# Kernel tuning notes

Hardware: AMD Instinct MI355X
Metric: run time of the kernel (lower is better)

Reference implementation:

```python
import jax, jax.numpy as jnp
import numpy as np

MODES = 32
NUM_BLOCKS = 4
NUM_EXPERTS = 16
TOP_K = 4
TEMPERATURE = 2.0


def _gelu(t):
    return jax.nn.gelu(t, approximate=False)  # torch F.gelu default (erf)


def _c1(x, w, b):
    # 1x1 conv: x [B,C,H,W], w [O,C], b [O]
    return jnp.einsum('bchw,oc->bohw', x, w) + b[None, :, None, None]


def _group_norm(x, w, b, groups=8, eps=1e-5):
    B, C, H, W = x.shape
    xg = x.reshape(B, groups, C // groups, H, W)
    mu = xg.mean(axis=(2, 3, 4), keepdims=True)
    var = xg.var(axis=(2, 3, 4), keepdims=True)
    xn = ((xg - mu) * jax.lax.rsqrt(var + eps)).reshape(B, C, H, W)
    return xn * w[None, :, None, None] + b[None, :, None, None]


def _bn_eval(x, g, b, rm, rv, eps=1e-5):
    # eval-mode BatchNorm with running stats
    return (x - rm) * jax.lax.rsqrt(rv + eps) * g + b


def _afno(x, w1, b1, w2, b2):
    # x: [B,C,H,W] (channel_first). Block-diagonal complex MLP on low FFT modes.
    B, C, H, W = x.shape
    bs = C // NUM_BLOCKS
    xp = x.transpose(0, 2, 3, 1)                      # [B,H,W,C]
    xf = jnp.fft.rfft2(xp, axes=(1, 2), norm='ortho') # [B,H,Wf,C] complex64
    Wf = xf.shape[2]
    xf = xf.reshape(B, H, Wf, NUM_BLOCKS, bs)
    m = MODES
    xm = xf[:, :m, :m]                                # kept modes only
    xr, xi = xm.real, xm.imag
    o1r = _gelu(jnp.einsum('bhwni,nio->bhwno', xr, w1[0])
                - jnp.einsum('bhwni,nio->bhwno', xi, w1[1]) + b1[0])
    o1i = _gelu(jnp.einsum('bhwni,nio->bhwno', xi, w1[0])
                + jnp.einsum('bhwni,nio->bhwno', xr, w1[1]) + b1[1])
    o2r = (jnp.einsum('bhwni,nio->bhwno', o1r, w2[0])
           - jnp.einsum('bhwni,nio->bhwno', o1i, w2[1]) + b2[0])
    o2i = (jnp.einsum('bhwni,nio->bhwno', o1i, w2[0])
           + jnp.einsum('bhwni,nio->bhwno', o1r, w2[1]) + b2[1])
    of = jnp.zeros((B, H, Wf, NUM_BLOCKS, bs), dtype=xf.dtype)
    of = of.at[:, :m, :m].set(o2r + 1j * o2i)
    out = jnp.fft.irfft2(of.reshape(B, H, Wf, C), s=(H, W), axes=(1, 2), norm='ortho')
    out = out + xp
    return out.transpose(0, 3, 1, 2)


def _forward(x, gn1_w, gn1_b, afno_w1, afno_b1, afno_w2, afno_b2,
             gn2_w, gn2_b, fe_w, fe_b, g1_w, g1_b, bn1_g, bn1_b, bn1_rm, bn1_rv,
             ca_w1, ca_b1, ca_w2, ca_b2, g2_w, g2_b, bn2_g, bn2_b, bn2_rm, bn2_rv,
             g3_w, g3_b, shared_w, shared_b, expert_w, expert_b):
    residual = x
    h = _group_norm(x, gn1_w, gn1_b)
    h = _afno(h, afno_w1, afno_b1, afno_w2, afno_b2)
    h = h + residual            # double_skip
    residual = h
    h = _group_norm(h, gn2_w, gn2_b)
    # MoEImage (eval mode -> loss_gate = 0)
    feats = _gelu(_c1(h, fe_w, fe_b))
    shared = jnp.zeros_like(h)
    for s in range(shared_w.shape[0]):
        shared = shared + _gelu(_c1(feats, shared_w[s], shared_b[s])) / shared_w.shape[0]
    # gating on global-avg-pooled features (1x1 convs == linears)
    gf = feats.mean(axis=(2, 3))                              # [B,C]
    h1 = _gelu(_bn_eval(gf @ g1_w.T + g1_b, bn1_g, bn1_b, bn1_rm, bn1_rv))
    a = _gelu(h1 @ ca_w1.T + ca_b1) @ ca_w2.T + ca_b2
    h1 = h1 * jax.nn.sigmoid(2.0 * a)                          # avg==max pool on 1x1 map
    h2 = _gelu(_bn_eval(h1 @ g2_w.T + g2_b, bn2_g, bn2_b, bn2_rm, bn2_rv))
    scores = h2 @ g3_w.T + g3_b                                # [B,E]
    vals, idx = jax.lax.top_k(scores, TOP_K)
    wts = jax.nn.softmax(vals / TEMPERATURE, axis=1)
    B = x.shape[0]
    gate_w = jnp.zeros((B, NUM_EXPERTS), x.dtype).at[jnp.arange(B)[:, None], idx].add(wts)
    out = shared
    for e in range(NUM_EXPERTS):
        out = out + _gelu(_c1(feats, expert_w[e], expert_b[e])) * gate_w[:, e][:, None, None, None]
    return out + residual


def setup_inputs():
    key = jax.random.key(0)
    ks = jax.random.split(key, 16)
    B, C, H, W = 8, 64, 192, 192
    nb = NUM_BLOCKS
    bs = C // nb
    E = NUM_EXPERTS
    scale = 1.0 / (bs * bs)
    f32 = jnp.float32
    n = lambda k, shape: jax.random.normal(k, shape, f32) * 0.02
    return {
        'x': jax.random.normal(ks[0], (B, C, H, W), f32),
        'gn1_w': jnp.ones((C,), f32), 'gn1_b': jnp.zeros((C,), f32),
        'afno_w1': jax.random.uniform(ks[1], (2, nb, bs, bs), f32) * scale,
        'afno_b1': jax.random.uniform(ks[2], (2, nb, bs), f32) * scale,
        'afno_w2': jax.random.uniform(ks[3], (2, nb, bs, bs), f32) * scale,
        'afno_b2': jax.random.uniform(ks[4], (2, nb, bs), f32) * scale,
        'gn2_w': jnp.ones((C,), f32), 'gn2_b': jnp.zeros((C,), f32),
        'fe_w': n(ks[5], (C, C)), 'fe_b': jnp.zeros((C,), f32),
        'g1_w': n(ks[6], (2 * C, C)), 'g1_b': jnp.zeros((2 * C,), f32),
        'bn1_g': jnp.ones((2 * C,), f32), 'bn1_b': jnp.zeros((2 * C,), f32),
        'bn1_rm': jnp.zeros((2 * C,), f32), 'bn1_rv': jnp.ones((2 * C,), f32),
        'ca_w1': n(ks[7], (2 * C // 16, 2 * C)), 'ca_b1': jnp.zeros((2 * C // 16,), f32),
        'ca_w2': n(ks[8], (2 * C, 2 * C // 16)), 'ca_b2': jnp.zeros((2 * C,), f32),
        'g2_w': n(ks[9], (C, 2 * C)), 'g2_b': jnp.zeros((C,), f32),
        'bn2_g': jnp.ones((C,), f32), 'bn2_b': jnp.zeros((C,), f32),
        'bn2_rm': jnp.zeros((C,), f32), 'bn2_rv': jnp.ones((C,), f32),
        'g3_w': n(ks[10], (E, C)), 'g3_b': jnp.zeros((E,), f32),
        'shared_w': n(ks[11], (2, C, C)), 'shared_b': jnp.zeros((2, C), f32),
        'expert_w': n(ks[12], (E, C, C)), 'expert_b': jnp.zeros((E, C), f32),
    }


def reference(x, gn1_w, gn1_b, afno_w1, afno_b1, afno_w2, afno_b2,
              gn2_w, gn2_b, fe_w, fe_b, g1_w, g1_b, bn1_g, bn1_b, bn1_rm, bn1_rv,
              ca_w1, ca_b1, ca_w2, ca_b2, g2_w, g2_b, bn2_g, bn2_b, bn2_rm, bn2_rv,
              g3_w, g3_b, shared_w, shared_b, expert_w, expert_b):
    return _forward(x, gn1_w, gn1_b, afno_w1, afno_b1, afno_w2, afno_b2,
                    gn2_w, gn2_b, fe_w, fe_b, g1_w, g1_b, bn1_g, bn1_b, bn1_rm, bn1_rv,
                    ca_w1, ca_b1, ca_w2, ca_b2, g2_w, g2_b, bn2_g, bn2_b, bn2_rm, bn2_rv,
                    g3_w, g3_b, shared_w, shared_b, expert_w, expert_b)
```

## Files before the change

kernel.cpp:

```cpp
#include <hip/hip_runtime.h>
#include <math.h>

#define TPI 6.283185307179586f

typedef __attribute__((ext_vector_type(8))) short bf8v;
typedef __attribute__((ext_vector_type(4))) float f4v;

#define MFMA(a,b,c) __builtin_amdgcn_mfma_f32_16x16x32_bf16((a),(b),(c),0,0,0)

__device__ __forceinline__ float gelu_f(float v){
  return 0.5f*v*(1.0f+erff(v*0.7071067811865475f));
}
__device__ __forceinline__ float gelu_fast(float x){
  float x3=x*x*x;
  float y=fmaf(0.044715f,x3,x)*0.7978845608f;
  float e=__expf(2.0f*y);
  float th=1.0f-2.0f/(e+1.0f);
  return 0.5f*x*(1.0f+th);
}
__device__ __forceinline__ unsigned short f2b(float f){
  union{float f; unsigned u;} v; v.f=f;
  unsigned r=v.u + 0x7FFFu + ((v.u>>16)&1u);
  return (unsigned short)(r>>16);
}

__global__ __launch_bounds__(256) void prep(const float* __restrict__ shw, const float* __restrict__ exw,
    const float* __restrict__ shb, const float* __restrict__ exb, const float* __restrict__ few,
    unsigned short* __restrict__ T, unsigned short* __restrict__ wall, float* __restrict__ ball,
    unsigned short* __restrict__ wfe, float* __restrict__ gfp){
  const float a = TPI/192.0f;
  int stride=gridDim.x*256;
  for(int i=blockIdx.x*256+threadIdx.x; i<61440; i+=stride){
    float v;
    if(i<12288){
      int n1=i/192, w=i%192; int kw=n1>>1, c=n1&1;
      int m=(kw*w)%192; float cs,sn; sincosf((float)m*a,&sn,&cs);
      v = c ? -sn : cs;
    } else if(i<36864){
      int j=i-12288; int n1=j/384, k1=j%384; int kh=n1>>1, d=n1&1; int h=k1>>1, c=k1&1;
      int m=(kh*h)%192; float cs,sn; sincosf((float)m*a,&sn,&cs);
      float e = d ? (c ? cs : -sn) : (c ? sn : cs);
      v = e*(1.0f/192.0f);
    } else if(i<49152){
      int j=i-36864; int h=j/64, k1=j%64; int kh=k1>>1, c=k1&1;
      int m=(h*kh)%192; float cs,sn; sincosf((float)m*a,&sn,&cs);
      v = c ? sn : cs;
    } else {
      int j=i-49152; int w=j/64, k1=j%64; int kw=k1>>1, d=k1&1;
      float f = kw ? (2.0f/192.0f) : (1.0f/192.0f);
      int m=(w*kw)%192; float cs,sn; sincosf((float)m*a,&sn,&cs);
      v = d ? -f*sn : f*cs;
    }
    T[i]=f2b(v);
  }
  for(int i=blockIdx.x*256+threadIdx.x;i<73728;i+=stride) wall[i]=f2b(i<8192?shw[i]:exw[i-8192]);
  for(int i=blockIdx.x*256+threadIdx.x;i<1152;i+=stride)  ball[i]=(i<128)?shb[i]:exb[i-128];
  for(int i=blockIdx.x*256+threadIdx.x;i<4096;i+=stride)  wfe[i]=f2b(few[i]);
  for(int i=blockIdx.x*256+threadIdx.x;i<512;i+=stride)   gfp[i]=0.f;
}

__global__ void gn_finalize(const float* __restrict__ part, const float* __restrict__ gw,
                            const float* __restrict__ gb, float2* __restrict__ sb){
  int g=threadIdx.x; if(g>=64) return;
  float S=0,SS=0;
  for(int j=0;j<8;j++){ S+=part[(g*8+j)*2]; SS+=part[(g*8+j)*2+1]; }
  const float inv=1.0f/294912.0f;
  float mean=S*inv, var=SS*inv-mean*mean;
  float rstd=rsqrtf(var+1e-5f);
  int b=g>>3, gg=g&7;
  for(int k=0;k<8;k++){
    int c=gg*8+k;
    float sc=rstd*gw[c];
    sb[b*64+c]=make_float2(sc, gb[c]-mean*sc);
  }
}

__global__ __launch_bounds__(256) void fwd_dft(const float* __restrict__ x,
      const unsigned short* __restrict__ TBf1, const unsigned short* __restrict__ TBf2,
      float* __restrict__ Xm2, float* __restrict__ part1){
  __shared__ __align__(16) unsigned short ldsA[64*200];
  __shared__ __align__(16) float sX[2048];
  __shared__ float red[8];
  int t=threadIdx.x, bc=blockIdx.x;
  int wave=t>>6, l=t&63, lr=l&15, lg=l>>4;
  const float* xch = x + (size_t)bc*36864;
  for(int i=t;i<1536;i+=256){
    int row=i/24, chunk=i%24;
    *(uint4*)&ldsA[row*200 + chunk*8] = *(const uint4*)(TBf1 + row*192 + chunk*8);
  }
  __syncthreads();
  float s_=0.f, ss_=0.f;
  f4v acc1[3][4];
  for(int mt=0;mt<3;mt++){
    int m0=(wave+mt*4)*16;
    const float* xrow = xch + (m0+lr)*192 + lg*8;
    bf8v af[6];
    #pragma unroll
    for(int ks=0;ks<6;ks++){
      float4 u0=*(const float4*)(xrow+ks*32);
      float4 u1=*(const float4*)(xrow+ks*32+4);
      s_ += u0.x+u0.y+u0.z+u0.w+u1.x+u1.y+u1.z+u1.w;
      ss_+= u0.x*u0.x+u0.y*u0.y+u0.z*u0.z+u0.w*u0.w
           +u1.x*u1.x+u1.y*u1.y+u1.z*u1.z+u1.w*u1.w;
      bf8v a;
      a[0]=(short)f2b(u0.x); a[1]=(short)f2b(u0.y); a[2]=(short)f2b(u0.z); a[3]=(short)f2b(u0.w);
      a[4]=(short)f2b(u1.x); a[5]=(short)f2b(u1.y); a[6]=(short)f2b(u1.z); a[7]=(short)f2b(u1.w);
      af[ks]=a;
    }
    #pragma unroll
    for(int nt=0;nt<4;nt++){
      f4v acc={0.f,0.f,0.f,0.f};
      #pragma unroll
      for(int ks=0;ks<6;ks++){
        bf8v b=*(const bf8v*)&ldsA[(nt*16+lr)*200 + ks*32 + lg*8];
        acc=MFMA(af[ks],b,acc);
      }
      acc1[mt][nt]=acc;
    }
  }
  __syncthreads();
  for(int mt=0;mt<3;mt++){
    int m0=(wave+mt*4)*16;
    #pragma unroll
    for(int nt=0;nt<4;nt++){
      int n1=nt*16+lr; int kw=n1>>1, c=n1&1;
      #pragma unroll
      for(int reg=0;reg<4;reg++){
        int h=m0+4*lg+reg;
        ldsA[kw*392 + 2*h + c]=f2b(acc1[mt][nt][reg]);
      }
    }
  }
  __syncthreads();
  for(int pp=0;pp<2;pp++){
    int p=wave+pp*4;
    int m0=(p>>2)*16, n0=(p&3)*16;
    f4v acc={0.f,0.f,0.f,0.f};
    #pragma unroll
    for(int ks=0;ks<12;ks++){
      bf8v a=*(const bf8v*)&ldsA[(m0+lr)*392 + ks*32 + lg*8];
      bf8v b=*(const bf8v*)(TBf2 + (n0+lr)*384 + ks*32 + lg*8);
      acc=MFMA(a,b,acc);
    }
    int n1=n0+lr; int kh=n1>>1, d=n1&1;
    #pragma unroll
    for(int reg=0;reg<4;reg++){
      int kw=m0+4*lg+reg;
      sX[(kh*32+kw)*2 + d]=acc[reg];
    }
  }
  __syncthreads();
  float* dst=Xm2+(size_t)bc*2048;
  for(int i=t;i<512;i+=256) *(float4*)(dst+i*4)=*(const float4*)(sX+i*4);
  #pragma unroll
  for(int o=32;o>0;o>>=1){ s_+=__shfl_down(s_,o); ss_+=__shfl_down(ss_,o); }
  if(l==0){ red[wave]=s_; red[4+wave]=ss_; }
  __syncthreads();
  if(t==0){
    part1[bc*2]  =red[0]+red[1]+red[2]+red[3];
    part1[bc*2+1]=red[4]+red[5]+red[6]+red[7];
  }
}

__global__ __launch_bounds__(256) void mode_mlp(const float* __restrict__ Xm2, const float2* __restrict__ sb1,
    const float* __restrict__ w1, const float* __restrict__ b1,
    const float* __restrict__ w2, const float* __restrict__ b2,
    float* __restrict__ S2){
  __shared__ float w10[1024], w11[1024], w20[1024], w21[1024];
  __shared__ float b10[64], b11[64], b20[64], b21[64];
  __shared__ float2 sbl[64];
  __shared__ float xr[32][64], xi[32][64];
  __shared__ float o1r[32][64], o1i[32][64];
  int t=threadIdx.x;
  int b=blockIdx.x>>5, kh=blockIdx.x&31;
  for(int i=t;i<1024;i+=256){ w10[i]=w1[i]; w11[i]=w1[1024+i]; w20[i]=w2[i]; w21[i]=w2[1024+i]; }
  if(t<64){ b10[t]=b1[t]; b11[t]=b1[64+t]; b20[t]=b2[t]; b21[t]=b2[64+t]; sbl[t]=sb1[b*64+t]; }
  __syncthreads();
  for(int q=0;q<16;q++){
    int idx=q*256+t; int c=idx>>6, jj=idx&63;
    float2 s=sbl[c];
    float v=Xm2[((size_t)(b*64+c))*2048 + kh*64 + jj]*s.x;
    if(kh==0 && jj==0) v += 192.0f*s.y;
    if(jj&1) xi[jj>>1][c]=v; else xr[jj>>1][c]=v;
  }
  __syncthreads();
  int tl=t&63, n=tl>>4, o=tl&15, wb=n*256+o;
  #pragma unroll
  for(int it=0;it<8;it++){
    int kw=(t>>6)+it*4;
    float a_r=b10[tl], a_i=b11[tl];
    #pragma unroll
    for(int i=0;i<16;i++){
      float rr=xr[kw][n*16+i], im=xi[kw][n*16+i];
      float W0=w10[wb+i*16], W1=w11[wb+i*16];
      a_r=fmaf(rr,W0,fmaf(-im,W1,a_r));
      a_i=fmaf(im,W0,fmaf( rr,W1,a_i));
    }
    o1r[kw][tl]=gelu_f(a_r); o1i[kw][tl]=gelu_f(a_i);
  }
  __syncthreads();
  #pragma unroll
  for(int it=0;it<8;it++){
    int kw=(t>>6)+it*4;
    float c_r=b20[tl], c_i=b21[tl];
    #pragma unroll
    for(int i=0;i<16;i++){
      float rr=o1r[kw][n*16+i], im=o1i[kw][n*16+i];
      float W0=w20[wb+i*16], W1=w21[wb+i*16];
      c_r=fmaf(rr,W0,fmaf(-im,W1,c_r));
      c_i=fmaf(im,W0,fmaf( rr,W1,c_i));
    }
    xr[kw][tl]=c_r; xi[kw][tl]=c_i;
  }
  __syncthreads();
  for(int q=0;q<16;q++){
    int idx=q*256+t; int c=idx>>6, jj=idx&63;
    float v = (jj&1) ? xi[jj>>1][c] : xr[jj>>1][c];
    S2[((size_t)(b*64+c))*2048 + kh*64 + jj]=v;
  }
}

__global__ __launch_bounds__(256) void inv_dft(const float* __restrict__ S2,
      const unsigned short* __restrict__ TAi, const unsigned short* __restrict__ TBi,
      const float* __restrict__ x, const float2* __restrict__ sb,
      float* __restrict__ h2, float* __restrict__ part2){
  __shared__ __align__(16) unsigned short Bs[64*72];
  __shared__ __align__(16) unsigned short GL[192*72];
  __shared__ float red[8];
  int t=threadIdx.x, bc=blockIdx.x;
  int wave=t>>6, l=t&63, lr=l&15, lg=l>>4;
  const float* sp=S2+(size_t)bc*2048;
  for(int i=t;i<1024;i+=256){
    int kh=i>>5, kw=i&31;
    float Sr=sp[(kh*32+kw)*2], Si=sp[(kh*32+kw)*2+1];
    unsigned short br=f2b(Sr), bi_=f2b(Si), nbi=f2b(-Si);
    Bs[(2*kw+0)*72 + 2*kh+0]=br;
    Bs[(2*kw+0)*72 + 2*kh+1]=nbi;
    Bs[(2*kw+1)*72 + 2*kh+0]=bi_;
    Bs[(2*kw+1)*72 + 2*kh+1]=br;
  }
  __syncthreads();
  for(int mt=0;mt<3;mt++){
    int m0=(wave+mt*4)*16;
    bf8v a0=*(const bf8v*)(TAi + (m0+lr)*64 + lg*8);
    bf8v a1=*(const bf8v*)(TAi + (m0+lr)*64 + 32 + lg*8);
    #pragma unroll
    for(int nt=0;nt<4;nt++){
      f4v acc={0.f,0.f,0.f,0.f};
      bf8v b0=*(const bf8v*)&Bs[(nt*16+lr)*72 + lg*8];
      bf8v b1=*(const bf8v*)&Bs[(nt*16+lr)*72 + 32 + lg*8];
      acc=MFMA(a0,b0,acc); acc=MFMA(a1,b1,acc);
      #pragma unroll
      for(int reg=0;reg<4;reg++)
        GL[(m0+4*lg+reg)*72 + nt*16+lr]=f2b(acc[reg]);
    }
  }
  __syncthreads();
  float2 sv=sb[bc];
  float cA=sv.x+1.0f, cB=sv.y;
  asm volatile("" : "+v"(cA), "+v"(cB));
  const float* xch=x+(size_t)bc*36864;
  float* och=h2+(size_t)bc*36864;
  float s_=0.f, ss_=0.f;
  for(int mt=0;mt<3;mt++){
    int m0=(wave+mt*4)*16;
    bf8v a0=*(const bf8v*)&GL[(m0+lr)*72 + lg*8];
    bf8v a1=*(const bf8v*)&GL[(m0+lr)*72 + 32 + lg*8];
    for(int nt=0;nt<12;nt++){
      int n0=nt*16;
      f4v acc={0.f,0.f,0.f,0.f};
      bf8v b0=*(const bf8v*)(TBi + (n0+lr)*64 + lg*8);
      bf8v b1=*(const bf8v*)(TBi + (n0+lr)*64 + 32 + lg*8);
      acc=MFMA(a0,b0,acc); acc=MFMA(a1,b1,acc);
      int w=n0+lr;
      #pragma unroll
      for(int reg=0;reg<4;reg++){
        int h=m0+4*lg+reg;
        int ga=h*192+w;
        float xv=xch[ga];
        float val=acc[reg]+fmaf(cA,xv,cB);
        och[ga]=val;
        s_+=val; ss_+=val*val;
      }
    }
  }
  #pragma unroll
  for(int o=32;o>0;o>>=1){ s_+=__shfl_down(s_,o); ss_+=__shfl_down(ss_,o); }
  if(l==0){ red[wave]=s_; red[4+wave]=ss_; }
  __syncthreads();
  if(t==0){
    part2[bc*2]  =red[0]+red[1]+red[2]+red[3];
    part2[bc*2+1]=red[4]+red[5]+red[6]+red[7];
  }
}

__global__ __launch_bounds__(256) void feats_k(const float* __restrict__ h2, const float2* __restrict__ sb,
    const unsigned short* __restrict__ wfe, const float* __restrict__ feb,
    unsigned short* __restrict__ feats, float* __restrict__ gfp){
  __shared__ __align__(16) unsigned short A[128*72];
  __shared__ float sgf[64];
  int t=threadIdx.x;
  int blk=blockIdx.x, b=blk/288, tile=blk-b*288, hw0=tile*128;
  if(t<64) sgf[t]=0.f;
  for(int i=t;i<2048;i+=256){
    int c=i>>5, q=i&31;
    float2 s=sb[b*64+c];
    float4 v=*(const float4*)&h2[(size_t)(b*64+c)*36864 + hw0 + q*4];
    int px0=q*4, sw=((px0>>4)&3)<<3, cc=c^sw;
    A[(px0+0)*72+cc]=f2b(fmaf(v.x,s.x,s.y));
    A[(px0+1)*72+cc]=f2b(fmaf(v.y,s.x,s.y));
    A[(px0+2)*72+cc]=f2b(fmaf(v.z,s.x,s.y));
    A[(px0+3)*72+cc]=f2b(fmaf(v.w,s.x,s.y));
  }
  __syncthreads();
  int wave=t>>6, l=t&63, lr=l&15, lg=l>>4;
  int pxb=wave*32;
  bf8v af[2][2], bfv[4][2];
  #pragma unroll
  for(int fm=0;fm<2;fm++){
    int row=pxb+fm*16+lr, sw=((row>>4)&3)<<3;
    #pragma unroll
    for(int ks=0;ks<2;ks++) af[fm][ks]=*(const bf8v*)&A[row*72+((ks*32+lg*8)^sw)];
  }
  #pragma unroll
  for(int fn=0;fn<4;fn++)
    #pragma unroll
    for(int ks=0;ks<2;ks++)
      bfv[fn][ks]=*(const bf8v*)(wfe+(fn*16+lr)*64+ks*32+lg*8);
  float gsum[4]={0.f,0.f,0.f,0.f};
  #pragma unroll
  for(int fm=0;fm<2;fm++)
    #pragma unroll
    for(int fn=0;fn<4;fn++){
      f4v acc={0.f,0.f,0.f,0.f};
      acc=MFMA(af[fm][0],bfv[fn][0],acc);
      acc=MFMA(af[fm][1],bfv[fn][1],acc);
      int oc=fn*16+lr;
      float bs=feb[oc];
      #pragma unroll
      for(int r=0;r<4;r++){
        float g=gelu_f(acc[r]+bs);
        gsum[fn]+=g;
        int px=hw0+pxb+fm*16+4*lg+r;
        feats[(size_t)(b*36864+px)*64+oc]=f2b(g);
      }
    }
  #pragma unroll
  for(int fn=0;fn<4;fn++){
    float v=gsum[fn];
    v+=__shfl_xor(v,16); v+=__shfl_xor(v,32);
    if(lg==0) atomicAdd(&sgf[fn*16+lr], v);
  }
  __syncthreads();
  if(t<64) atomicAdd(&gfp[b*64+t], sgf[t]);
}

__global__ __launch_bounds__(128) void gating(const float* __restrict__ gfp,
  const float* __restrict__ g1w, const float* __restrict__ g1b,
  const float* __restrict__ bn1g, const float* __restrict__ bn1b, const float* __restrict__ bn1m, const float* __restrict__ bn1v,
  const float* __restrict__ cw1, const float* __restrict__ cb1, const float* __restrict__ cw2, const float* __restrict__ cb2,
  const float* __restrict__ g2w, const float* __restrict__ g2b,
  const float* __restrict__ bn2g, const float* __restrict__ bn2b, const float* __restrict__ bn2m, const float* __restrict__ bn2v,
  const float* __restrict__ g3w, const float* __restrict__ g3b, float2* __restrict__ act){
  __shared__ float gf[8][64];
  __shared__ float h1[8][128];
  __shared__ float a1[8][8];
  __shared__ float h2g[8][64];
  __shared__ float sc[8][16];
  int t=threadIdx.x;
  for(int i=t;i<512;i+=128) gf[i>>6][i&63]=gfp[i]*(1.0f/36864.0f);
  __syncthreads();
  for(int i=t;i<1024;i+=128){
    int b=i>>7, j=i&127;
    float s=g1b[j];
    for(int c=0;c<64;c++) s=fmaf(gf[b][c], g1w[j*64+c], s);
    s=(s-bn1m[j])*rsqrtf(bn1v[j]+1e-5f)*bn1g[j]+bn1b[j];
    h1[b][j]=gelu_f(s);
  }
  __syncthreads();
  if(t<64){
    int b=t>>3, k=t&7; float s=cb1[k];
    for(int j=0;j<128;j++) s=fmaf(h1[b][j], cw1[k*128+j], s);
    a1[b][k]=gelu_f(s);
  }
  __syncthreads();
  for(int i=t;i<1024;i+=128){
    int b=i>>7, j=i&127;
    float s=cb2[j];
    for(int k=0;k<8;k++) s=fmaf(a1[b][k], cw2[j*8+k], s);
    h1[b][j]=h1[b][j]/(1.0f+expf(-2.0f*s));
  }
  __syncthreads();
  for(int i=t;i<512;i+=128){
    int b=i>>6, j=i&63;
    float s=g2b[j];
    for(int k=0;k<128;k++) s=fmaf(h1[b][k], g2w[j*128+k], s);
    s=(s-bn2m[j])*rsqrtf(bn2v[j]+1e-5f)*bn2g[j]+bn2b[j];
    h2g[b][j]=gelu_f(s);
  }
  __syncthreads();
  {
    int b=t>>4, e=t&15;
    float s=g3b[e];
    for(int c=0;c<64;c++) s=fmaf(h2g[b][c], g3w[e*64+c], s);
    sc[b][e]=s;
  }
  __syncthreads();
  if(t<8){
    int b=t;
    float v[16];
    for(int e=0;e<16;e++) v[e]=sc[b][e];
    float vals[4]; int idx[4];
    for(int k=0;k<4;k++){
      float best=-1e30f; int bi=0;
      for(int e=0;e<16;e++) if(v[e]>best){best=v[e];bi=e;}
      vals[k]=best; idx[k]=bi; v[bi]=-1e30f;
    }
    float m=vals[0], ssum=0.f, w[4];
    for(int k=0;k<4;k++){ w[k]=expf((vals[k]-m)*0.5f); ssum+=w[k]; }
    act[b*6+0]=make_float2(0.5f, __int_as_float(0));
    act[b*6+1]=make_float2(0.5f, __int_as_float(1));
    for(int k=0;k<4;k++) act[b*6+2+k]=make_float2(w[k]/ssum, __int_as_float(2+idx[k]));
  }
}

__global__ __launch_bounds__(256) void final_k(const unsigned short* __restrict__ feats,
  const unsigned short* __restrict__ wall, const float* __restrict__ ball,
  const float2* __restrict__ act, float* __restrict__ out){
  __shared__ __align__(16) unsigned short A[128*72];
  int t=threadIdx.x;
  int blk=blockIdx.x, b=blk/288, tile=blk-b*288, hw0=tile*128;
  for(int i=t;i<1024;i+=256){
    int px=i>>3, c0=(i&7)*8, sw=((px>>4)&3)<<3;
    *(uint4*)&A[px*72+(c0^sw)]=*(const uint4*)&feats[(size_t)(b*36864+hw0+px)*64+c0];
  }
  __syncthreads();
  int wave=t>>6, l=t&63, lr=l&15, lg=l>>4;
  int pxb=wave*32;
  bf8v af[2][2];
  #pragma unroll
  for(int fm=0;fm<2;fm++){
    int row=pxb+fm*16+lr, sw=((row>>4)&3)<<3;
    #pragma unroll
    for(int ks=0;ks<2;ks++) af[fm][ks]=*(const bf8v*)&A[row*72+((ks*32+lg*8)^sw)];
  }
  float oa[2][4][4]={};
  #pragma unroll 2
  for(int j=0;j<6;j++){
    float2 aw=act[b*6+j];
    int term=__float_as_int(aw.y);
    float g=aw.x;
    const unsigned short* wp=wall+term*4096;
    const float* bp=ball+term*64;
    bf8v bfv[4][2];
    #pragma unroll
    for(int fn=0;fn<4;fn++)
      #pragma unroll
      for(int ks=0;ks<2;ks++)
        bfv[fn][ks]=*(const bf8v*)(wp+(fn*16+lr)*64+ks*32+lg*8);
    #pragma unroll
    for(int fm=0;fm<2;fm++)
      #pragma unroll
      for(int fn=0;fn<4;fn++){
        f4v acc={0.f,0.f,0.f,0.f};
        acc=MFMA(af[fm][0],bfv[fn][0],acc);
        acc=MFMA(af[fm][1],bfv[fn][1],acc);
        float bs=bp[fn*16+lr];
        #pragma unroll
        for(int r=0;r<4;r++)
          oa[fm][fn][r]=fmaf(g, gelu_fast(acc[r]+bs), oa[fm][fn][r]);
      }
  }
  float* Fo=(float*)A;
  #pragma unroll
  for(int half=0;half<2;half++){
    __syncthreads();
    #pragma unroll
    for(int fm=0;fm<2;fm++)
      #pragma unroll
      for(int fn2=0;fn2<2;fn2++){
        int fn=half*2+fn2;
        int ocl=fn2*16+lr;
        *(float4*)&Fo[ocl*132 + pxb + fm*16 + 4*lg] =
            make_float4(oa[fm][fn][0],oa[fm][fn][1],oa[fm][fn][2],oa[fm][fn][3]);
      }
    __syncthreads();
    for(int i=t;i<1024;i+=256){
      int ocl=i>>5, px0=(i&31)*4;
      int oc=half*32+ocl;
      size_t base=(size_t)(b*64+oc)*36864 + hw0 + px0;
      float4 rv=*(const float4*)&out[base];
      float4 ov=*(const float4*)&Fo[ocl*132+px0];
      *(float4*)&out[base]=make_float4(ov.x+rv.x,ov.y+rv.y,ov.z+rv.z,ov.w+rv.w);
    }
  }
}

extern "C" void kernel_launch(void* const* d_in, const int* in_sizes, int n_in,
                              void* d_out, int out_size, void* d_ws, size_t ws_size,
                              hipStream_t stream){
  const float* x    =(const float*)d_in[0];
  const float* gn1w =(const float*)d_in[1];
  const float* gn1b =(const float*)d_in[2];
  const float* aw1  =(const float*)d_in[3];
  const float* ab1  =(const float*)d_in[4];
  const float* aw2  =(const float*)d_in[5];
  const float* ab2  =(const float*)d_in[6];
  const float* gn2w =(const float*)d_in[7];
  const float* gn2b =(const float*)d_in[8];
  const float* few  =(const float*)d_in[9];
  const float* feb  =(const float*)d_in[10];
  const float* g1w  =(const float*)d_in[11];
  const float* g1b  =(const float*)d_in[12];
  const float* bn1g =(const float*)d_in[13];
  const float* bn1b =(const float*)d_in[14];
  const float* bn1m =(const float*)d_in[15];
  const float* bn1v =(const float*)d_in[16];
  const float* cw1  =(const float*)d_in[17];
  const float* cb1  =(const float*)d_in[18];
  const float* cw2  =(const float*)d_in[19];
  const float* cb2  =(const float*)d_in[20];
  const float* g2w  =(const float*)d_in[21];
  const float* g2b  =(const float*)d_in[22];
  const float* bn2g =(const float*)d_in[23];
  const float* bn2b =(const float*)d_in[24];
  const float* bn2m =(const float*)d_in[25];
  const float* bn2v =(const float*)d_in[26];
  const float* g3w  =(const float*)d_in[27];
  const float* g3b  =(const float*)d_in[28];
  const float* shw  =(const float*)d_in[29];
  const float* shb  =(const float*)d_in[30];
  const float* exw  =(const float*)d_in[31];
  const float* exb  =(const float*)d_in[32];

  float* out=(float*)d_out;
  float* ws=(float*)d_ws;

  float*  part1 = ws;
  float*  part2 = ws+1024;
  float2* sb1   = (float2*)(ws+2048);
  float2* sb2   = (float2*)(ws+3072);
  float2* act   = (float2*)(ws+4096);
  float*  gfp   = ws+4224;
  float*  Xm2   = ws+8192;
  float*  S2    = ws+1056768;
  unsigned short* Tbl  = (unsigned short*)(ws+2105344);
  unsigned short* wall = (unsigned short*)(ws+2136064);
  float*          ball = ws+2172928;
  unsigned short* wfe  = (unsigned short*)(ws+2174080);
  unsigned short* feats= (unsigned short*)(ws+2176128);
  const unsigned short* TBf1 = Tbl;
  const unsigned short* TBf2 = Tbl+12288;
  const unsigned short* TAi  = Tbl+36864;
  const unsigned short* TBi  = Tbl+49152;

  prep<<<64,256,0,stream>>>(shw, exw, shb, exb, few, Tbl, wall, ball, wfe, gfp);
  fwd_dft <<<512,256,0,stream>>>(x, TBf1, TBf2, Xm2, part1);
  gn_finalize<<<1,64,0,stream>>>(part1, gn1w, gn1b, sb1);
  mode_mlp<<<256,256,0,stream>>>(Xm2, sb1, aw1, ab1, aw2, ab2, S2);
  inv_dft <<<512,256,0,stream>>>(S2, TAi, TBi, x, sb1, out, part2);
  gn_finalize<<<1,64,0,stream>>>(part2, gn2w, gn2b, sb2);
  feats_k<<<2304,256,0,stream>>>(out, sb2, wfe, feb, feats, gfp);
  gating <<<1,128,0,stream>>>(gfp, g1w,g1b, bn1g,bn1b,bn1m,bn1v,
                              cw1,cb1,cw2,cb2, g2w,g2b, bn2g,bn2b,bn2m,bn2v,
                              g3w,g3b, act);
  final_k<<<2304,256,0,stream>>>(feats, wall, ball, act, out);
}
```

Measured before the change: 243.2 us.

## Recompute expert input features inside final kernel instead of storing bf16 feats

The feature-extraction kernel now only accumulates the pooled gating sums and no longer writes a bf16 per-pixel feature tensor. The final kernel reloads the normalized h2 tile, redoes the feature 1x1 conv with MFMA, and stages the results through shared memory before the expert MFMAs. This removes the scattered 2-byte feats stores and the later feats reload. The cost is a second full fp32 read of h2 plus duplicated MFMA and GELU work. The features now use the tanh-approximate GELU instead of the erf one, and gelu_fast is rewritten with fewer operations and a hardware reciprocal, which slightly changes numerics.

```diff
diff --git a/kernel.cpp b/kernel.cpp
--- a/kernel.cpp
+++ b/kernel.cpp
@@ -12,11 +12,11 @@
   return 0.5f*v*(1.0f+erff(v*0.7071067811865475f));
 }
 __device__ __forceinline__ float gelu_fast(float x){
-  float x3=x*x*x;
-  float y=fmaf(0.044715f,x3,x)*0.7978845608f;
-  float e=__expf(2.0f*y);
-  float th=1.0f-2.0f/(e+1.0f);
-  return 0.5f*x*(1.0f+th);
+  float x2=x*x;
+  float inner=fmaf(0.044715f*x2, x, x);
+  float e=__expf(1.5957691216057308f*inner);
+  float r=__builtin_amdgcn_rcpf(1.0f+e);
+  return fmaf(-x, r, x);
 }
 __device__ __forceinline__ unsigned short f2b(float f){
   union{float f; unsigned u;} v; v.f=f;
@@ -294,9 +294,9 @@
   }
 }
 
-__global__ __launch_bounds__(256) void feats_k(const float* __restrict__ h2, const float2* __restrict__ sb,
+__global__ __launch_bounds__(256) void gf_k(const float* __restrict__ h2, const float2* __restrict__ sb,
     const unsigned short* __restrict__ wfe, const float* __restrict__ feb,
-    unsigned short* __restrict__ feats, float* __restrict__ gfp){
+    float* __restrict__ gfp){
   __shared__ __align__(16) unsigned short A[128*72];
   __shared__ float sgf[64];
   int t=threadIdx.x;
@@ -335,15 +335,9 @@
       f4v acc={0.f,0.f,0.f,0.f};
       acc=MFMA(af[fm][0],bfv[fn][0],acc);
       acc=MFMA(af[fm][1],bfv[fn][1],acc);
-      int oc=fn*16+lr;
-      float bs=feb[oc];
-      #pragma unroll
-      for(int r=0;r<4;r++){
-        float g=gelu_f(acc[r]+bs);
-        gsum[fn]+=g;
-        int px=hw0+pxb+fm*16+4*lg+r;
-        feats[(size_t)(b*36864+px)*64+oc]=f2b(g);
-      }
+      float bs=feb[fn*16+lr];
+      #pragma unroll
+      for(int r=0;r<4;r++) gsum[fn]+=gelu_f(acc[r]+bs);
     }
   #pragma unroll
   for(int fn=0;fn<4;fn++){
@@ -424,25 +418,69 @@
   }
 }
 
-__global__ __launch_bounds__(256) void final_k(const unsigned short* __restrict__ feats,
+__global__ __launch_bounds__(256) void final_k(const float* __restrict__ h2, const float2* __restrict__ sb,
+  const unsigned short* __restrict__ wfe, const float* __restrict__ feb,
   const unsigned short* __restrict__ wall, const float* __restrict__ ball,
   const float2* __restrict__ act, float* __restrict__ out){
   __shared__ __align__(16) unsigned short A[128*72];
   int t=threadIdx.x;
   int blk=blockIdx.x, b=blk/288, tile=blk-b*288, hw0=tile*128;
-  for(int i=t;i<1024;i+=256){
-    int px=i>>3, c0=(i&7)*8, sw=((px>>4)&3)<<3;
-    *(uint4*)&A[px*72+(c0^sw)]=*(const uint4*)&feats[(size_t)(b*36864+hw0+px)*64+c0];
+  for(int i=t;i<2048;i+=256){
+    int c=i>>5, q=i&31;
+    float2 s=sb[b*64+c];
+    float4 v=*(const float4*)&h2[(size_t)(b*64+c)*36864 + hw0 + q*4];
+    int px0=q*4, sw=((px0>>4)&3)<<3, cc=c^sw;
+    A[(px0+0)*72+cc]=f2b(fmaf(v.x,s.x,s.y));
+    A[(px0+1)*72+cc]=f2b(fmaf(v.y,s.x,s.y));
+    A[(px0+2)*72+cc]=f2b(fmaf(v.z,s.x,s.y));
+    A[(px0+3)*72+cc]=f2b(fmaf(v.w,s.x,s.y));
   }
   __syncthreads();
   int wave=t>>6, l=t&63, lr=l&15, lg=l>>4;
   int pxb=wave*32;
-  bf8v af[2][2];
+  bf8v af[2][2], bfe[4][2];
   #pragma unroll
   for(int fm=0;fm<2;fm++){
     int row=pxb+fm*16+lr, sw=((row>>4)&3)<<3;
     #pragma unroll
     for(int ks=0;ks<2;ks++) af[fm][ks]=*(const bf8v*)&A[row*72+((ks*32+lg*8)^sw)];
+  }
+  #pragma unroll
+  for(int fn=0;fn<4;fn++)
+    #pragma unroll
+    for(int ks=0;ks<2;ks++)
+      bfe[fn][ks]=*(const bf8v*)(wfe+(fn*16+lr)*64+ks*32+lg*8);
+  unsigned short pf[2][4][4];
+  #pragma unroll
+  for(int fm=0;fm<2;fm++)
+    #pragma unroll
+    for(int fn=0;fn<4;fn++){
+      f4v acc={0.f,0.f,0.f,0.f};
+      acc=MFMA(af[fm][0],bfe[fn][0],acc);
+      acc=MFMA(af[fm][1],bfe[fn][1],acc);
+      float bs=feb[fn*16+lr];
+      #pragma unroll
+      for(int r=0;r<4;r++) pf[fm][fn][r]=f2b(gelu_fast(acc[r]+bs));
+    }
+  __syncthreads();
+  #pragma unroll
+  for(int fm=0;fm<2;fm++){
+    int sw=(((pxb+fm*16)>>4)&3)<<3;
+    #pragma unroll
+    for(int fn=0;fn<4;fn++){
+      int cc=(fn*16+lr)^sw;
+      #pragma unroll
+      for(int r=0;r<4;r++)
+        A[(pxb+fm*16+4*lg+r)*72+cc]=pf[fm][fn][r];
+    }
+  }
+  __syncthreads();
+  bf8v af2[2][2];
+  #pragma unroll
+  for(int fm=0;fm<2;fm++){
+    int row=pxb+fm*16+lr, sw=((row>>4)&3)<<3;
+    #pragma unroll
+    for(int ks=0;ks<2;ks++) af2[fm][ks]=*(const bf8v*)&A[row*72+((ks*32+lg*8)^sw)];
   }
   float oa[2][4][4]={};
   #pragma unroll 2
@@ -463,8 +501,8 @@
       #pragma unroll
       for(int fn=0;fn<4;fn++){
         f4v acc={0.f,0.f,0.f,0.f};
-        acc=MFMA(af[fm][0],bfv[fn][0],acc);
-        acc=MFMA(af[fm][1],bfv[fn][1],acc);
+        acc=MFMA(af2[fm][0],bfv[fn][0],acc);
+        acc=MFMA(af2[fm][1],bfv[fn][1],acc);
         float bs=bp[fn*16+lr];
         #pragma unroll
         for(int r=0;r<4;r++)
@@ -548,7 +586,6 @@
   unsigned short* wall = (unsigned short*)(ws+2136064);
   float*          ball = ws+2172928;
   unsigned short* wfe  = (unsigned short*)(ws+2174080);
-  unsigned short* feats= (unsigned short*)(ws+2176128);
   const unsigned short* TBf1 = Tbl;
   const unsigned short* TBf2 = Tbl+12288;
   const unsigned short* TAi  = Tbl+36864;
@@ -560,9 +597,9 @@
   mode_mlp<<<256,256,0,stream>>>(Xm2, sb1, aw1, ab1, aw2, ab2, S2);
   inv_dft <<<512,256,0,stream>>>(S2, TAi, TBi, x, sb1, out, part2);
   gn_finalize<<<1,64,0,stream>>>(part2, gn2w, gn2b, sb2);
-  feats_k<<<2304,256,0,stream>>>(out, sb2, wfe, feb, feats, gfp);
+  gf_k<<<2304,256,0,stream>>>(out, sb2, wfe, feb, gfp);
   gating <<<1,128,0,stream>>>(gfp, g1w,g1b, bn1g,bn1b,bn1m,bn1v,
                               cw1,cb1,cw2,cb2, g2w,g2b, bn2g,bn2b,bn2m,bn2v,
                               g3w,g3b, act);
-  final_k<<<2304,256,0,stream>>>(feats, wall, ball, act, out);
-}
+  final_k<<<2304,256,0,stream>>>(out, sb2, wfe, feb, wall, ball, act, out);
+}
```

Measured after the change: 238.7 us. No clear change (-1.8%).
